# Kernel tuning notes

Measured on AMD Instinct MI355X. Metric: run time of the kernel, lower is better.

## Reference

```python
import jax, jax.numpy as jnp
import numpy as np
from jax import lax

GAMMA = 1.0
B = 10            # forced by qnn_arch[0]=10 via w1 @ x in feedforward
N_TRAIN = 8192    # kernel support set size


def setup_inputs() -> dict:
    key = jax.random.key(0)
    ks = jax.random.split(key, 20)
    x = jax.random.normal(ks[0], (B, 3, 250, 250), jnp.float32)
    # CNN params (He-ish scale)
    conv1_w = jax.random.normal(ks[1], (6, 3, 5, 5), jnp.float32) * 0.1
    conv1_b = jax.random.normal(ks[2], (6,), jnp.float32) * 0.01
    conv2_w = jax.random.normal(ks[3], (15, 6, 3, 3), jnp.float32) * 0.1
    conv2_b = jax.random.normal(ks[4], (15,), jnp.float32) * 0.01
    fc1_w = jax.random.normal(ks[5], (120, 55815), jnp.float32) * 0.004
    fc1_b = jax.random.normal(ks[6], (120,), jnp.float32) * 0.01
    fc2_w = jax.random.normal(ks[7], (84, 120), jnp.float32) * 0.09
    fc2_b = jax.random.normal(ks[8], (84,), jnp.float32) * 0.01
    fc3_w = jax.random.normal(ks[9], (1, 84), jnp.float32) * 0.1
    fc3_b = jax.random.normal(ks[10], (1,), jnp.float32) * 0.01
    # QNN weights (original uses plain randn)
    qnn_w1 = jax.random.normal(ks[11], (20, 10), jnp.float32)
    qnn_w2 = jax.random.normal(ks[12], (5, 20), jnp.float32)
    # Precomputed training states: tanh(w2 @ tanh(w1 @ f)) per random feature f
    feats = jax.random.normal(ks[13], (N_TRAIN, 10), jnp.float32)
    train_states = jnp.tanh(jnp.tanh(feats @ qnn_w1.T) @ qnn_w2.T)  # [N_TRAIN, 5]
    kcls_w = jax.random.normal(ks[14], (2, N_TRAIN), jnp.float32) * 0.01
    kcls_b = jax.random.normal(ks[15], (2,), jnp.float32) * 0.01
    return {
        'x': x,
        'conv1_w': conv1_w, 'conv1_b': conv1_b,
        'conv2_w': conv2_w, 'conv2_b': conv2_b,
        'fc1_w': fc1_w, 'fc1_b': fc1_b,
        'fc2_w': fc2_w, 'fc2_b': fc2_b,
        'fc3_w': fc3_w, 'fc3_b': fc3_b,
        'qnn_w1': qnn_w1, 'qnn_w2': qnn_w2,
        'train_states': train_states,
        'kcls_w': kcls_w, 'kcls_b': kcls_b,
    }


def _conv(h, w, b, stride, pad):
    out = lax.conv_general_dilated(
        h, w, (stride, stride), [(pad, pad), (pad, pad)],
        dimension_numbers=('NCHW', 'OIHW', 'NCHW'))
    return out + b[None, :, None, None]


def _maxpool_2s1(h):
    return lax.reduce_window(h, -jnp.inf, lax.max, (1, 1, 2, 2), (1, 1, 1, 1), 'VALID')


def reference(x, conv1_w, conv1_b, conv2_w, conv2_b, fc1_w, fc1_b,
              fc2_w, fc2_b, fc3_w, fc3_b, qnn_w1, qnn_w2,
              train_states, kcls_w, kcls_b):
    h = jax.nn.relu(_conv(x, conv1_w, conv1_b, 2, 1))   # [10,6,124,124]
    h = _maxpool_2s1(h)                                 # [10,6,123,123]
    h = jax.nn.relu(_conv(h, conv2_w, conv2_b, 2, 1))   # [10,15,62,62]
    h = _maxpool_2s1(h)                                 # [10,15,61,61]
    h = h.reshape(h.shape[0], -1)                       # [10,55815]
    h = jax.nn.relu(h @ fc1_w.T + fc1_b)                # [10,120]
    h = jax.nn.relu(h @ fc2_w.T + fc2_b)                # [10,84]
    h = h @ fc3_w.T + fc3_b                             # [10,1]
    # QNN feedforward: batch dim B=10 is consumed as the qnn input dim
    s = jnp.tanh(qnn_w1 @ h)                            # [20,1]
    s = jnp.tanh(qnn_w2 @ s)                            # [5,1]
    fs = s[:, 0]                                        # [5]
    # Batched RBF kernel against all train states (replaces the Python .item() loop)
    d2 = jnp.sum((fs[None, :] - train_states) ** 2, axis=-1)  # [N_TRAIN]
    K = jnp.exp(-GAMMA * d2)                            # [N_TRAIN]
    out = K[None, :] @ kcls_w.T + kcls_b                # [1,2]
    return out
```

## Files before the change

kernel.cpp:

```cpp
#include <hip/hip_runtime.h>


#define ACT_STRIDE 55816

__global__ __launch_bounds__(256) void convpool1_k(
    const float* __restrict__ x, const float* __restrict__ w,
    const float* __restrict__ bias, float* __restrict__ out ) {
    const int b   = blockIdx.x;
    const int py0 = blockIdx.y * 4;
    const int px0 = blockIdx.z * 62;
    const int n_py = (123 - py0) < 4 ? (123 - py0) : 4;
    const int n_oy = n_py + 1;
    const int iy0 = 2 * py0 - 1;
    const int ix0 = 2 * px0 - 1;

    __shared__ float sx[3][13][132];
    __shared__ float so[6][5][64];

    const int tid = threadIdx.x;

    for (int j = tid; j < 3 * 13 * 129; j += 256) {
        int c  = j % 129;
        int r  = (j / 129) % 13;
        int ic = j / (129 * 13);
        int ix = ix0 + c, iy = iy0 + r;
        float v = 0.f;
        if ((unsigned)ix < 250u && (unsigned)iy < 250u)
            v = x[((size_t)(b * 3 + ic) * 250 + iy) * 250 + ix];
        sx[ic][r][c] = v;
    }
    __syncthreads();

    for (int p = tid; p < n_oy * 63; p += 256) {
        int oxl = p % 63;
        int oyl = p / 63;
        if (px0 + oxl < 124) {
            float acc[6];
            #pragma unroll
            for (int o = 0; o < 6; ++o) acc[o] = bias[o];
            #pragma unroll
            for (int ic = 0; ic < 3; ++ic) {
                #pragma unroll
                for (int ky = 0; ky < 5; ++ky) {
                    const float* xr = &sx[ic][2 * oyl + ky][2 * oxl];
                    #pragma unroll
                    for (int kx = 0; kx < 5; ++kx) {
                        float xv = xr[kx];
                        #pragma unroll
                        for (int o = 0; o < 6; ++o)
                            acc[o] += w[((o * 3 + ic) * 5 + ky) * 5 + kx] * xv;
                    }
                }
            }
            #pragma unroll
            for (int o = 0; o < 6; ++o) so[o][oyl][oxl] = fmaxf(acc[o], 0.f);
        }
    }
    __syncthreads();

    for (int j = tid; j < 6 * 4 * 62; j += 256) {
        int pxl = j % 62;
        int pyl = (j / 62) & 3;
        int oc  = j / 248;
        int px = px0 + pxl, py = py0 + pyl;
        if (pyl < n_py && px < 123) {
            float v = fmaxf(fmaxf(so[oc][pyl][pxl],     so[oc][pyl][pxl + 1]),
                            fmaxf(so[oc][pyl + 1][pxl], so[oc][pyl + 1][pxl + 1]));
            out[((size_t)(b * 6 + oc) * 123 + py) * 123 + px] = v;
        }
    }
}

__global__ __launch_bounds__(128) void convpool2_k(
    const float* __restrict__ in , const float* __restrict__ w,
    const float* __restrict__ bias, float* __restrict__ out ) {
    const int b   = blockIdx.x;
    const int py0 = blockIdx.y * 2;
    const int px0 = blockIdx.z * 31;
    const int n_py = (61 - py0) < 2 ? (61 - py0) : 2;
    const int n_oy = n_py + 1;
    const int iy0 = 2 * py0 - 1;
    const int ix0 = 2 * px0 - 1;

    __shared__ float sx[6][7][68];
    __shared__ float so[15][3][32];

    const int tid = threadIdx.x;

    for (int j = tid; j < 6 * 7 * 65; j += 128) {
        int col = j % 65;
        int r   = (j / 65) % 7;
        int ic  = j / (65 * 7);
        int ix = ix0 + col, iy = iy0 + r;
        float v = 0.f;
        if ((unsigned)ix < 123u && (unsigned)iy < 123u)
            v = in[((size_t)(b * 6 + ic) * 123 + iy) * 123 + ix];
        sx[ic][r][col] = v;
    }
    __syncthreads();

    for (int p = tid; p < n_oy * 32; p += 128) {
        int oxl = p & 31;
        int oyl = p >> 5;
        if (px0 + oxl < 62) {
            float acc[15];
            #pragma unroll
            for (int o = 0; o < 15; ++o) acc[o] = bias[o];
            #pragma unroll
            for (int ic = 0; ic < 6; ++ic) {
                #pragma unroll
                for (int ky = 0; ky < 3; ++ky) {
                    const float* xr = &sx[ic][2 * oyl + ky][2 * oxl];
                    #pragma unroll
                    for (int kx = 0; kx < 3; ++kx) {
                        float xv = xr[kx];
                        #pragma unroll
                        for (int o = 0; o < 15; ++o)
                            acc[o] += w[((o * 6 + ic) * 3 + ky) * 3 + kx] * xv;
                    }
                }
            }
            #pragma unroll
            for (int o = 0; o < 15; ++o) so[o][oyl][oxl] = fmaxf(acc[o], 0.f);
        }
    }
    __syncthreads();

    for (int j = tid; j < 15 * 2 * 31; j += 128) {
        int pxl = j % 31;
        int pyl = (j / 31) & 1;
        int oc  = j / 62;
        int px = px0 + pxl, py = py0 + pyl;
        if (pyl < n_py && px < 61) {
            float v = fmaxf(fmaxf(so[oc][pyl][pxl],     so[oc][pyl][pxl + 1]),
                            fmaxf(so[oc][pyl + 1][pxl], so[oc][pyl + 1][pxl + 1]));
            out[(size_t)b * ACT_STRIDE + ((size_t)oc * 61 + py) * 61 + px] = v;
        }
    }
}

#define FC1_K      55815
#define FC1_CHUNK  768
#define FC1_NC     73
#define FC1_RT     15

__global__ __launch_bounds__(256) void fc1_partial_k(
    const float* __restrict__ act ,
    const float* __restrict__ w   ,
    float* __restrict__ partials  ) {
    int rt  = blockIdx.x;
    int c   = blockIdx.y;
    int tid = threadIdx.x;
    int wave = tid >> 6, lane = tid & 63;
    int k0 = c * FC1_CHUNK;
    int k1 = k0 + FC1_CHUNK; if (k1 > FC1_K) k1 = FC1_K;
    int r0 = rt * 8 + wave * 2;
    const float* w0 = w + (size_t)r0 * FC1_K;
    const float* w1 = w + (size_t)(r0 + 1) * FC1_K;

    float acc0[10], acc1[10];
    #pragma unroll
    for (int b = 0; b < 10; ++b) { acc0[b] = 0.f; acc1[b] = 0.f; }

    for (int k = k0 + lane * 4; k < k1; k += 256) {
        if (k + 4 <= k1) {
            float4 a4[10];
            #pragma unroll
            for (int b = 0; b < 10; ++b)
                a4[b] = *reinterpret_cast<const float4*>(act + (size_t)b * ACT_STRIDE + k);
            float w00 = w0[k], w01 = w0[k + 1], w02 = w0[k + 2], w03 = w0[k + 3];
            float w10 = w1[k], w11 = w1[k + 1], w12 = w1[k + 2], w13 = w1[k + 3];
            #pragma unroll
            for (int b = 0; b < 10; ++b) {
                acc0[b] += w00 * a4[b].x + w01 * a4[b].y + w02 * a4[b].z + w03 * a4[b].w;
                acc1[b] += w10 * a4[b].x + w11 * a4[b].y + w12 * a4[b].z + w13 * a4[b].w;
            }
        } else {
            for (int j = 0; j < k1 - k; ++j) {
                float wv0 = w0[k + j], wv1 = w1[k + j];
                #pragma unroll
                for (int b = 0; b < 10; ++b) {
                    float av = act[(size_t)b * ACT_STRIDE + k + j];
                    acc0[b] += wv0 * av;
                    acc1[b] += wv1 * av;
                }
            }
        }
    }
    #pragma unroll
    for (int b = 0; b < 10; ++b) {
        float v0 = acc0[b], v1 = acc1[b];
        for (int off = 32; off > 0; off >>= 1) {
            v0 += __shfl_down(v0, off);
            v1 += __shfl_down(v1, off);
        }
        if (lane == 0) {
            size_t base = ((size_t)c * 120 + r0) * 10;
            partials[base + b]      = v0;
            partials[base + 10 + b] = v1;
        }
    }
}

__global__ __launch_bounds__(128) void fcA_k(
    const float* __restrict__ part , const float* __restrict__ fc1_b,
    const float* __restrict__ fc2_w, const float* __restrict__ fc2_b,
    const float* __restrict__ fc3_w, const float* __restrict__ fc3_b,
    float* __restrict__ h3 ) {
    const int b = blockIdx.x;
    const int tid = threadIdx.x;
    __shared__ float s_act[120];
    __shared__ float s_fc2[84];

    if (tid < 120) {
        float s = 0.f;
        for (int c = 0; c < FC1_NC; ++c) s += part[((size_t)c * 120 + tid) * 10 + b];
        s_act[tid] = fmaxf(s + fc1_b[tid], 0.f);
    }
    __syncthreads();
    if (tid < 84) {
        float acc = fc2_b[tid];
        #pragma unroll 4
        for (int k = 0; k < 120; ++k) acc += s_act[k] * fc2_w[tid * 120 + k];
        s_fc2[tid] = fmaxf(acc, 0.f);
    }
    __syncthreads();
    if (tid < 64) {
        float v = s_fc2[tid] * fc3_w[tid];
        if (tid < 20) v += s_fc2[tid + 64] * fc3_w[tid + 64];
        for (int off = 32; off > 0; off >>= 1) v += __shfl_down(v, off);
        if (tid == 0) h3[b] = v + fc3_b[0];
    }
}

__global__ __launch_bounds__(128) void clsB_k(
    const float* __restrict__ h3 ,
    const float* __restrict__ qw1, const float* __restrict__ qw2,
    const float* __restrict__ ts , const float* __restrict__ kw ,
    float* __restrict__ partials ) {
    int tid = threadIdx.x;
    __shared__ float s_h3[10], s_s1[20], s_fs[5];
    if (tid < 10) s_h3[tid] = h3[tid];
    __syncthreads();
    if (tid < 20) {
        float acc = 0.f;
        for (int b = 0; b < 10; ++b) acc += qw1[tid * 10 + b] * s_h3[b];
        s_s1[tid] = tanhf(acc);
    }
    __syncthreads();
    if (tid < 5) {
        float acc = 0.f;
        for (int j = 0; j < 20; ++j) acc += qw2[tid * 20 + j] * s_s1[j];
        s_fs[tid] = tanhf(acc);
    }
    __syncthreads();

    float f0 = s_fs[0], f1 = s_fs[1], f2 = s_fs[2], f3 = s_fs[3], f4 = s_fs[4];
    int n = blockIdx.x * 128 + tid;
    const float* t = ts + (size_t)n * 5;
    float d0 = f0 - t[0], d1 = f1 - t[1], d2 = f2 - t[2], d3 = f3 - t[3], d4 = f4 - t[4];
    float Kv = expf(-(d0 * d0 + d1 * d1 + d2 * d2 + d3 * d3 + d4 * d4));
    float a0 = Kv * kw[n];
    float a1 = Kv * kw[8192 + n];
    for (int off = 32; off > 0; off >>= 1) {
        a0 += __shfl_down(a0, off);
        a1 += __shfl_down(a1, off);
    }
    __shared__ float l0[2], l1[2];
    int wave = tid >> 6, lane = tid & 63;
    if (lane == 0) { l0[wave] = a0; l1[wave] = a1; }
    __syncthreads();
    if (tid == 0) {
        partials[blockIdx.x * 2 + 0] = l0[0] + l0[1];
        partials[blockIdx.x * 2 + 1] = l1[0] + l1[1];
    }
}

__global__ void clsC_k(const float* __restrict__ partials,
                       const float* __restrict__ kb, float* __restrict__ out) {
    int c = threadIdx.x;
    if (c < 2) {
        float acc = kb[c];
        for (int i = 0; i < 64; ++i) acc += partials[i * 2 + c];
        out[c] = acc;
    }
}

extern "C" void kernel_launch(void* const* d_in, const int* in_sizes, int n_in,
                              void* d_out, int out_size, void* d_ws, size_t ws_size,
                              hipStream_t stream) {
    const float* x        = (const float*)d_in[0];
    const float* conv1_w  = (const float*)d_in[1];
    const float* conv1_b  = (const float*)d_in[2];
    const float* conv2_w  = (const float*)d_in[3];
    const float* conv2_b  = (const float*)d_in[4];
    const float* fc1_w    = (const float*)d_in[5];
    const float* fc1_b    = (const float*)d_in[6];
    const float* fc2_w    = (const float*)d_in[7];
    const float* fc2_b    = (const float*)d_in[8];
    const float* fc3_w    = (const float*)d_in[9];
    const float* fc3_b    = (const float*)d_in[10];
    const float* qnn_w1   = (const float*)d_in[11];
    const float* qnn_w2   = (const float*)d_in[12];
    const float* tstates  = (const float*)d_in[13];
    const float* kcls_w   = (const float*)d_in[14];
    const float* kcls_b   = (const float*)d_in[15];

    float* ws = (float*)d_ws;
    float* p1       = ws;
    float* p2       = p1 + 907740;
    float* fc1_part = p2 + 558160;
    float* h3       = fc1_part + 87600;
    float* partials = h3 + 16;

    convpool1_k<<<dim3(10, 31, 2), 256, 0, stream>>>(x, conv1_w, conv1_b, p1);
    convpool2_k<<<dim3(10, 31, 2), 128, 0, stream>>>(p1, conv2_w, conv2_b, p2);
    fc1_partial_k<<<dim3(FC1_RT, FC1_NC), 256, 0, stream>>>(p2, fc1_w, fc1_part);
    fcA_k<<<10, 128, 0, stream>>>(fc1_part, fc1_b, fc2_w, fc2_b, fc3_w, fc3_b, h3);
    clsB_k<<<64, 128, 0, stream>>>(h3, qnn_w1, qnn_w2, tstates, kcls_w, partials);
    clsC_k<<<1, 64, 0, stream>>>(partials, kcls_b, (float*)d_out);
}
```

Measured before the change: 80.93 us.

## Retile conv1 for one output per thread, register windows, finer fc1 split

Conv1 tiles shrink to 3 pooled rows by 63 columns, so each of the 256 threads computes exactly one conv output. The loop-stride and bounds logic go away, and the ReLU moves after the max-pool. Both conv kernels now load the input window into registers before the FMA loops. The fc1 K-chunk drops from 768 to 512, giving more blocks with less work each, at the cost of more partials to reduce in the next kernel. Smaller conv1 tiles also mean more halo reloads and more blocks.

```diff
diff --git a/kernel.cpp b/kernel.cpp
--- a/kernel.cpp
+++ b/kernel.cpp
@@ -7,22 +7,20 @@
     const float* __restrict__ x, const float* __restrict__ w,
     const float* __restrict__ bias, float* __restrict__ out ) {
     const int b   = blockIdx.x;
-    const int py0 = blockIdx.y * 4;
-    const int px0 = blockIdx.z * 62;
-    const int n_py = (123 - py0) < 4 ? (123 - py0) : 4;
-    const int n_oy = n_py + 1;
+    const int py0 = blockIdx.y * 3;
+    const int px0 = blockIdx.z * 63;
     const int iy0 = 2 * py0 - 1;
     const int ix0 = 2 * px0 - 1;
 
-    __shared__ float sx[3][13][132];
-    __shared__ float so[6][5][64];
+    __shared__ float sx[3][11][132];
+    __shared__ float so[6][4][64];
 
     const int tid = threadIdx.x;
 
-    for (int j = tid; j < 3 * 13 * 129; j += 256) {
-        int c  = j % 129;
-        int r  = (j / 129) % 13;
-        int ic = j / (129 * 13);
+    for (int j = tid; j < 3 * 11 * 131; j += 256) {
+        int c  = j % 131;
+        int r  = (j / 131) % 11;
+        int ic = j / (131 * 11);
         int ix = ix0 + c, iy = iy0 + r;
         float v = 0.f;
         if ((unsigned)ix < 250u && (unsigned)iy < 250u)
@@ -31,42 +29,44 @@
     }
     __syncthreads();
 
-    for (int p = tid; p < n_oy * 63; p += 256) {
-        int oxl = p % 63;
-        int oyl = p / 63;
-        if (px0 + oxl < 124) {
-            float acc[6];
-            #pragma unroll
-            for (int o = 0; o < 6; ++o) acc[o] = bias[o];
-            #pragma unroll
-            for (int ic = 0; ic < 3; ++ic) {
-                #pragma unroll
-                for (int ky = 0; ky < 5; ++ky) {
-                    const float* xr = &sx[ic][2 * oyl + ky][2 * oxl];
+    {
+        const int oxl = tid & 63;
+        const int oyl = tid >> 6;
+        float acc[6];
+        #pragma unroll
+        for (int o = 0; o < 6; ++o) acc[o] = bias[o];
+        #pragma unroll
+        for (int ic = 0; ic < 3; ++ic) {
+            float win[5][5];
+            #pragma unroll
+            for (int r = 0; r < 5; ++r)
+                #pragma unroll
+                for (int c = 0; c < 5; ++c)
+                    win[r][c] = sx[ic][2 * oyl + r][2 * oxl + c];
+            #pragma unroll
+            for (int r = 0; r < 5; ++r)
+                #pragma unroll
+                for (int c = 0; c < 5; ++c) {
+                    float xv = win[r][c];
                     #pragma unroll
-                    for (int kx = 0; kx < 5; ++kx) {
-                        float xv = xr[kx];
-                        #pragma unroll
-                        for (int o = 0; o < 6; ++o)
-                            acc[o] += w[((o * 3 + ic) * 5 + ky) * 5 + kx] * xv;
-                    }
+                    for (int o = 0; o < 6; ++o)
+                        acc[o] = fmaf(w[((o * 3 + ic) * 5 + r) * 5 + c], xv, acc[o]);
                 }
-            }
-            #pragma unroll
-            for (int o = 0; o < 6; ++o) so[o][oyl][oxl] = fmaxf(acc[o], 0.f);
-        }
-    }
-    __syncthreads();
-
-    for (int j = tid; j < 6 * 4 * 62; j += 256) {
-        int pxl = j % 62;
-        int pyl = (j / 62) & 3;
-        int oc  = j / 248;
+        }
+        #pragma unroll
+        for (int o = 0; o < 6; ++o) so[o][oyl][oxl] = acc[o];
+    }
+    __syncthreads();
+
+    for (int j = tid; j < 6 * 3 * 63; j += 256) {
+        int pxl = j % 63;
+        int pyl = (j / 63) % 3;
+        int oc  = j / 189;
         int px = px0 + pxl, py = py0 + pyl;
-        if (pyl < n_py && px < 123) {
+        if (px < 123) {
             float v = fmaxf(fmaxf(so[oc][pyl][pxl],     so[oc][pyl][pxl + 1]),
                             fmaxf(so[oc][pyl + 1][pxl], so[oc][pyl + 1][pxl + 1]));
-            out[((size_t)(b * 6 + oc) * 123 + py) * 123 + px] = v;
+            out[((size_t)(b * 6 + oc) * 123 + py) * 123 + px] = fmaxf(v, 0.f);
         }
     }
 }
@@ -108,16 +108,18 @@
             for (int o = 0; o < 15; ++o) acc[o] = bias[o];
             #pragma unroll
             for (int ic = 0; ic < 6; ++ic) {
-                #pragma unroll
-                for (int ky = 0; ky < 3; ++ky) {
-                    const float* xr = &sx[ic][2 * oyl + ky][2 * oxl];
+                float win[9];
+                #pragma unroll
+                for (int ky = 0; ky < 3; ++ky)
                     #pragma unroll
-                    for (int kx = 0; kx < 3; ++kx) {
-                        float xv = xr[kx];
-                        #pragma unroll
-                        for (int o = 0; o < 15; ++o)
-                            acc[o] += w[((o * 6 + ic) * 3 + ky) * 3 + kx] * xv;
-                    }
+                    for (int kx = 0; kx < 3; ++kx)
+                        win[ky * 3 + kx] = sx[ic][2 * oyl + ky][2 * oxl + kx];
+                #pragma unroll
+                for (int t = 0; t < 9; ++t) {
+                    float xv = win[t];
+                    #pragma unroll
+                    for (int o = 0; o < 15; ++o)
+                        acc[o] = fmaf(w[(o * 6 + ic) * 9 + t], xv, acc[o]);
                 }
             }
             #pragma unroll
@@ -140,8 +142,8 @@
 }
 
 #define FC1_K      55815
-#define FC1_CHUNK  768
-#define FC1_NC     73
+#define FC1_CHUNK  512
+#define FC1_NC     110
 #define FC1_RT     15
 
 __global__ __launch_bounds__(256) void fc1_partial_k(
@@ -310,10 +312,10 @@
     float* p1       = ws;
     float* p2       = p1 + 907740;
     float* fc1_part = p2 + 558160;
-    float* h3       = fc1_part + 87600;
+    float* h3       = fc1_part + 132000;
     float* partials = h3 + 16;
 
-    convpool1_k<<<dim3(10, 31, 2), 256, 0, stream>>>(x, conv1_w, conv1_b, p1);
+    convpool1_k<<<dim3(10, 41, 2), 256, 0, stream>>>(x, conv1_w, conv1_b, p1);
     convpool2_k<<<dim3(10, 31, 2), 128, 0, stream>>>(p1, conv2_w, conv2_b, p2);
     fc1_partial_k<<<dim3(FC1_RT, FC1_NC), 256, 0, stream>>>(p2, fc1_w, fc1_part);
     fcA_k<<<10, 128, 0, stream>>>(fc1_part, fc1_b, fc2_w, fc2_b, fc3_w, fc3_b, h3);
```

Result: slower. 84.06 us (+3.9%).
